# Kernel optimization log

Measured on AMD Instinct MI355X. Metric: run time of the kernel, lower is better.

The kernel has to match this reference:

```python
import jax, jax.numpy as jnp
import numpy as np

B, T, EMB, HS = 4, 4096, 1024, 64
BASE = 10000.0


def rope_angles(T, hs, base=BASE):
    # theta_i = base^(-2i/hs), freqs[t, i] = t * theta_i  -> (T, hs//2)
    inv = 1.0 / (base ** (2.0 * jnp.arange(hs // 2, dtype=jnp.float32) / hs))
    return jnp.arange(T, dtype=jnp.float32)[:, None] * inv[None, :]


def apply_rope(x, cos, sin):
    # x: (B, T, D); pairs are interleaved (even, odd) like torch.view_as_complex
    xr = x.reshape(*x.shape[:-1], -1, 2)
    xe, xo = xr[..., 0], xr[..., 1]
    re = xe * cos - xo * sin
    im = xe * sin + xo * cos
    return jnp.stack([re, im], axis=-1).reshape(x.shape)


def setup_inputs() -> dict:
    key = jax.random.key(0)
    kx, kq, kk, kv = jax.random.split(key, 4)
    s = 1.0 / np.sqrt(EMB)
    return {
        "x": jax.random.normal(kx, (B, T, EMB), jnp.float32),
        "Wq": jax.random.normal(kq, (HS, EMB), jnp.float32) * s,
        "Wk": jax.random.normal(kk, (HS, EMB), jnp.float32) * s,
        "Wv": jax.random.normal(kv, (HS, EMB), jnp.float32) * s,
    }


def reference(x, Wq, Wk, Wv):
    Tlen = x.shape[1]
    ang = rope_angles(Tlen, HS)          # (T, HS//2)
    cos, sin = jnp.cos(ang), jnp.sin(ang)
    q = x @ Wq.T                          # (B, T, HS)
    k = x @ Wk.T
    v = x @ Wv.T
    q = apply_rope(q, cos, sin)
    k = apply_rope(k, cos, sin)
    scores = jnp.einsum("bqd,bkd->bqk", q, k) * (HS ** -0.5)
    causal = jnp.tril(jnp.ones((Tlen, Tlen), dtype=bool))
    scores = jnp.where(causal[None], scores, -jnp.inf)
    w = jax.nn.softmax(scores, axis=-1)   # dropout in eval mode: identity
    return jnp.einsum("bqk,bkd->bqd", w, v)
```

## Files before the change

kernel.cpp:

```cpp
#include <hip/hip_runtime.h>

typedef __bf16 bf16x8 __attribute__((ext_vector_type(8)));
typedef __bf16 bf16x4 __attribute__((ext_vector_type(4)));
typedef float f32x4 __attribute__((ext_vector_type(4)));
typedef float f32x16 __attribute__((ext_vector_type(16)));
typedef unsigned int u32;

#define T_LEN 4096

__device__ __forceinline__ f32x4 mfma16(bf16x8 a, bf16x8 b, f32x4 c) {
    return __builtin_amdgcn_mfma_f32_16x16x32_bf16(a, b, c, 0, 0, 0);
}
__device__ __forceinline__ f32x16 mfma32(bf16x8 a, bf16x8 b, f32x16 c) {
    return __builtin_amdgcn_mfma_f32_32x32x16_bf16(a, b, c, 0, 0, 0);
}
__device__ __forceinline__ u32 packbf(float lo, float hi) {
    union { __bf16 e[2]; u32 w; } u;
    u.e[0] = (__bf16)lo; u.e[1] = (__bf16)hi;
    return u.w;
}
__device__ __forceinline__ f32x16 zero16() {
    f32x16 z;
    #pragma unroll
    for (int i = 0; i < 16; i++) z[i] = 0.f;
    return z;
}

__global__ __launch_bounds__(256) void convert_w_kernel(
    const float* __restrict__ Wq, const float* __restrict__ Wk,
    const float* __restrict__ Wv, __bf16* __restrict__ wb)
{
    int i = blockIdx.x * 256 + threadIdx.x;
    int m = i >> 14, off = (i & 16383) << 2;
    const float* s = (m == 0 ? Wq : (m == 1 ? Wk : Wv)) + off;
    float4 f = *(const float4*)s;
    bf16x4 h = { (__bf16)f.x, (__bf16)f.y, (__bf16)f.z, (__bf16)f.w };
    *(bf16x4*)(wb + (m << 16) + off) = h;
}

__global__ __launch_bounds__(512, 2) void proj_kernel(
    const float* __restrict__ x, const __bf16* __restrict__ wb,
    __bf16* __restrict__ qfb, __bf16* __restrict__ kfb, __bf16* __restrict__ vfb)
{
    __shared__ __bf16 xs[2][32][72];
    __shared__ __bf16 wl[2][192][72];
    const int tid  = threadIdx.x;
    const int wave = tid >> 6, lane = tid & 63;
    const int l15 = lane & 15, l4 = lane >> 4;
    const int wm = wave >> 2, wn = wave & 3;
    const size_t m0 = (size_t)blockIdx.x * 32;
    const int xrow = tid >> 4, xc4 = (tid & 15) * 4;
    const int wrow = tid >> 3, wcp = (tid & 7) * 8;

    f32x4 acc[3];
    #pragma unroll
    for (int bn = 0; bn < 3; bn++) acc[bn] = (f32x4){0.f, 0.f, 0.f, 0.f};

    const float* xsrc = x + (m0 + xrow) * 1024 + xc4;

    float4 rx;
    bf16x8 rw[3];

    rx = *(const float4*)(xsrc);
    #pragma unroll
    for (int j = 0; j < 3; j++)
        rw[j] = *(const bf16x8*)(wb + (size_t)(wrow + j * 64) * 1024 + wcp);
    {
        bf16x4 hx = {(__bf16)rx.x, (__bf16)rx.y, (__bf16)rx.z, (__bf16)rx.w};
        *(bf16x4*)&xs[0][xrow][xc4] = hx;
        #pragma unroll
        for (int j = 0; j < 3; j++)
            *(bf16x8*)&wl[0][wrow + j * 64][wcp] = rw[j];
    }
    __syncthreads();

    for (int t = 0; t < 16; t++) {
        const int cur = t & 1;
        if (t < 15) {
            const int k0 = (t + 1) * 64;
            rx = *(const float4*)(xsrc + k0);
            #pragma unroll
            for (int j = 0; j < 3; j++)
                rw[j] = *(const bf16x8*)(wb + (size_t)(wrow + j * 64) * 1024 + k0 + wcp);
        }
        bf16x8 af[2], bfr[3][2];
        #pragma unroll
        for (int c = 0; c < 2; c++)
            af[c] = *(const bf16x8*)&xs[cur][wm * 16 + l15][c * 32 + l4 * 8];
        #pragma unroll
        for (int nf = 0; nf < 3; nf++)
            #pragma unroll
            for (int c = 0; c < 2; c++)
                bfr[nf][c] = *(const bf16x8*)&wl[cur][wn * 48 + nf * 16 + l15][c * 32 + l4 * 8];
        #pragma unroll
        for (int nf = 0; nf < 3; nf++)
            #pragma unroll
            for (int c = 0; c < 2; c++)
                acc[nf] = mfma16(af[c], bfr[nf][c], acc[nf]);
        if (t < 15) {
            bf16x4 hx = {(__bf16)rx.x, (__bf16)rx.y, (__bf16)rx.z, (__bf16)rx.w};
            *(bf16x4*)&xs[cur ^ 1][xrow][xc4] = hx;
            #pragma unroll
            for (int j = 0; j < 3; j++)
                *(bf16x8*)&wl[cur ^ 1][wrow + j * 64][wcp] = rw[j];
        }
        __syncthreads();
    }

    #pragma unroll
    for (int nf = 0; nf < 3; nf++) {
        int n = wn * 48 + nf * 16 + l15;
        #pragma unroll
        for (int r = 0; r < 4; r++) {
            size_t mrow = m0 + wm * 16 + l4 * 4 + r;
            float val = acc[nf][r];
            float partner = __shfl_xor(val, 1);
            const int bb = (int)(mrow >> 12);
            const int tq = (int)(mrow & 4095);
            const size_t bbase = (size_t)bb * 262144;
            if (n < 128) {
                int i = (n & 63) >> 1;
                float inv = __builtin_exp2f((float)i * (-13.287712379549449f / 32.f));
                float ang = (float)tq * inv;
                float sn, cs;
                __sincosf(ang, &sn, &cs);
                float res = (n & 1) ? (partner * sn + val * cs)
                                    : (val * cs - partner * sn);
                if (n < 64) {
                    res *= 0.180336884f;
                    int d = n;
                    size_t idx = bbase + (size_t)(tq >> 5) * 2048 + (d >> 4) * 512
                               + ((tq & 31) + ((d >> 3) & 1) * 32) * 8 + (d & 7);
                    qfb[idx] = (__bf16)res;
                } else {
                    int d = n - 64, rr = tq & 31;
                    int l31i = ((rr >> 2) & 1) * 16 + ((rr >> 4) & 1) * 8
                             + ((rr >> 3) & 1) * 4 + (rr & 3);
                    size_t idx = bbase + (size_t)(tq >> 5) * 2048 + (d >> 4) * 512
                               + (l31i + ((d >> 3) & 1) * 32) * 8 + (d & 7);
                    kfb[idx] = (__bf16)res;
                }
            } else {
                int d = n - 128;
                int cc = ((d >> 5) << 1) | ((tq & 31) >> 4);
                size_t idx = bbase + (size_t)(tq >> 5) * 2048 + cc * 512
                           + ((d & 31) + ((tq >> 3) & 1) * 32) * 8 + (tq & 7);
                vfb[idx] = (__bf16)val;
            }
        }
    }
}

__global__ __launch_bounds__(1024) void flash_kernel(
    const __bf16* __restrict__ qfb, const __bf16* __restrict__ kfb,
    const __bf16* __restrict__ vfb, float* __restrict__ out)
{
    __shared__ float ods[16][32][36];
    __shared__ float mls[2][16][32];

    const int tid = threadIdx.x;
    const int wave = tid >> 6, lane = tid & 63;
    const int l31 = lane & 31, h = lane >> 5;
    const int xcd = blockIdx.x & 7;
    const int b = xcd >> 1;
    const int p = ((blockIdx.x >> 3) << 1) | (xcd & 1);

    const __bf16* qb_b = qfb + (size_t)b * 262144;
    const __bf16* kb_b = kfb + (size_t)b * 262144;
    const __bf16* vb_b = vfb + (size_t)b * 262144;

    #pragma unroll 1
    for (int half = 0; half < 2; half++) {
        const int jt = half ? p : 127 - p;
        const int q0 = jt * 32;
        const int qg = q0 + l31;

        const __bf16* qp = qb_b + (size_t)jt * 2048 + lane * 8;
        bf16x8 qf[4];
        #pragma unroll
        for (int dc = 0; dc < 4; dc++) qf[dc] = *(const bf16x8*)(qp + dc * 512);

        float m = 16.f, l = 0.f;
        f32x16 o0 = zero16(), o1 = zero16();
        const int nt = jt + 1;

        #pragma unroll 1
        for (int kt = wave; kt < nt; kt += 16) {
            const int kc0 = kt << 5;
            const __bf16* kr = kb_b + (size_t)kt * 2048 + lane * 8;
            bf16x8 kf0 = *(const bf16x8*)(kr);
            bf16x8 kf1 = *(const bf16x8*)(kr + 512);
            bf16x8 kf2 = *(const bf16x8*)(kr + 1024);
            bf16x8 kf3 = *(const bf16x8*)(kr + 1536);
            const __bf16* vr = vb_b + (size_t)kt * 2048 + lane * 8;
            bf16x8 vf00 = *(const bf16x8*)(vr);
            bf16x8 vf01 = *(const bf16x8*)(vr + 512);
            bf16x8 vf10 = *(const bf16x8*)(vr + 1024);
            bf16x8 vf11 = *(const bf16x8*)(vr + 1536);
            f32x16 s = zero16();
            __builtin_amdgcn_s_setprio(1);
            s = mfma32(kf0, qf[0], s);
            s = mfma32(kf1, qf[1], s);
            s = mfma32(kf2, qf[2], s);
            s = mfma32(kf3, qf[3], s);
            __builtin_amdgcn_s_setprio(0);
            if (kt == jt) {
                #pragma unroll
                for (int r = 0; r < 16; r++) {
                    int pioff = ((r >> 2) & 1) * 16 + 8 * h + (r >> 3) * 4 + (r & 3);
                    if (kc0 + pioff > qg) s[r] = -1e30f;
                }
            }
            float tm[8];
            #pragma unroll
            for (int i = 0; i < 8; i++) tm[i] = fmaxf(s[2 * i], s[2 * i + 1]);
            #pragma unroll
            for (int i = 0; i < 4; i++) tm[i] = fmaxf(tm[i], tm[i + 4]);
            float tmax = fmaxf(fmaxf(tm[0], tm[1]), fmaxf(tm[2], tm[3]));
            float ts[4] = {0.f, 0.f, 0.f, 0.f};
            #pragma unroll
            for (int r = 0; r < 16; r++) {
                float e = __builtin_exp2f(s[r] - m);
                s[r] = e;
                ts[r & 3] += e;
            }
            float lsum = (ts[0] + ts[1]) + (ts[2] + ts[3]);
            float lsum_p = __shfl_xor(lsum, 32);
            float tmax_p = __shfl_xor(tmax, 32);
            union { u32 w[4]; bf16x8 v; } pf[2];
            #pragma unroll
            for (int cg = 0; cg < 2; cg++) {
                pf[cg].w[0] = packbf(s[4 * cg + 0],  s[4 * cg + 1]);
                pf[cg].w[1] = packbf(s[4 * cg + 2],  s[4 * cg + 3]);
                pf[cg].w[2] = packbf(s[4 * cg + 8],  s[4 * cg + 9]);
                pf[cg].w[3] = packbf(s[4 * cg + 10], s[4 * cg + 11]);
            }
            __builtin_amdgcn_s_setprio(1);
            o0 = mfma32(vf00, pf[0].v, o0);
            o0 = mfma32(vf01, pf[1].v, o0);
            o1 = mfma32(vf10, pf[0].v, o1);
            o1 = mfma32(vf11, pf[1].v, o1);
            __builtin_amdgcn_s_setprio(0);
            l += lsum + lsum_p;
            float tmx = fmaxf(tmax, tmax_p);
            if (!__all(tmx <= m + 8.f)) {
                const float mnew = fmaxf(m, tmx);
                const float alpha = __builtin_exp2f(m - mnew);
                m = mnew;
                l *= alpha;
                #pragma unroll
                for (int r = 0; r < 16; r++) { o0[r] *= alpha; o1[r] *= alpha; }
            }
        }

        const int q = tid >> 5, dcm = tid & 31;
        #pragma unroll
        for (int c2 = 0; c2 < 4; c2++) {
            f32x4 w0 = {o0[4 * c2], o0[4 * c2 + 1], o0[4 * c2 + 2], o0[4 * c2 + 3]};
            *(f32x4*)&ods[wave][l31][8 * c2 + 4 * h] = w0;
        }
        if (h == 0) {
            mls[0][wave][l31] = (wave < nt) ? m : -1e30f;
            mls[1][wave][l31] = l;
        }
        __syncthreads();
        float M = -1e30f;
        #pragma unroll
        for (int s2 = 0; s2 < 16; s2++) M = fmaxf(M, mls[0][s2][q]);
        float w16[16], L = 0.f;
        #pragma unroll
        for (int s2 = 0; s2 < 16; s2++) {
            float ws = __builtin_exp2f(mls[0][s2][q] - M);
            w16[s2] = ws;
            L += ws * mls[1][s2][q];
        }
        const float invL = 1.f / L;
        float accA = 0.f;
        #pragma unroll
        for (int s2 = 0; s2 < 16; s2++) accA += w16[s2] * ods[s2][q][dcm];
        out[((size_t)b * T_LEN + q0 + q) * 64 + dcm] = accA * invL;
        __syncthreads();
        #pragma unroll
        for (int c2 = 0; c2 < 4; c2++) {
            f32x4 w1 = {o1[4 * c2], o1[4 * c2 + 1], o1[4 * c2 + 2], o1[4 * c2 + 3]};
            *(f32x4*)&ods[wave][l31][8 * c2 + 4 * h] = w1;
        }
        __syncthreads();
        float accB = 0.f;
        #pragma unroll
        for (int s2 = 0; s2 < 16; s2++) accB += w16[s2] * ods[s2][q][dcm];
        out[((size_t)b * T_LEN + q0 + q) * 64 + 32 + dcm] = accB * invL;
        __syncthreads();
    }
}

extern "C" void kernel_launch(void* const* d_in, const int* in_sizes, int n_in,
                              void* d_out, int out_size, void* d_ws, size_t ws_size,
                              hipStream_t stream)
{
    const float* x  = (const float*)d_in[0];
    const float* Wq = (const float*)d_in[1];
    const float* Wk = (const float*)d_in[2];
    const float* Wv = (const float*)d_in[3];
    float* out = (float*)d_out;

    __bf16* qfb = (__bf16*)d_ws;
    __bf16* kfb = qfb + 1048576;
    __bf16* vfb = kfb + 1048576;
    __bf16* wb  = vfb + 1048576;

    convert_w_kernel<<<192, 256, 0, stream>>>(Wq, Wk, Wv, wb);
    proj_kernel<<<512, 512, 0, stream>>>(x, wb, qfb, kfb, vfb);
    flash_kernel<<<256, 1024, 0, stream>>>(qfb, kfb, vfb, out);
}
```

Measured before the change: 62.49 us.

## Stage projection outputs in LDS for vectorized stores; deepen x prefetch

The projection kernel now writes its rotated Q/K and V values into a shared-memory staging buffer, which reuses the tile buffers. After a barrier, each thread copies them to global memory as contiguous 4-element bf16 stores, replacing scattered 2-byte stores. The x loads are also prefetched two k-steps ahead instead of one, to hide more global latency. The cost is an extra barrier, extra register pressure from the second prefetch register, and some index arithmetic.

```diff
diff --git a/kernel.cpp b/kernel.cpp
--- a/kernel.cpp
+++ b/kernel.cpp
@@ -42,8 +42,11 @@
     const float* __restrict__ x, const __bf16* __restrict__ wb,
     __bf16* __restrict__ qfb, __bf16* __restrict__ kfb, __bf16* __restrict__ vfb)
 {
-    __shared__ __bf16 xs[2][32][72];
-    __shared__ __bf16 wl[2][192][72];
+    __shared__ __bf16 smem[4608 + 27648];
+    __bf16 (*xs)[32][72]  = (__bf16(*)[32][72])smem;
+    __bf16 (*wl)[192][72] = (__bf16(*)[192][72])(smem + 4608);
+    __bf16* stage = smem;
+
     const int tid  = threadIdx.x;
     const int wave = tid >> 6, lane = tid & 63;
     const int l15 = lane & 15, l4 = lane >> 4;
@@ -58,27 +61,28 @@
 
     const float* xsrc = x + (m0 + xrow) * 1024 + xc4;
 
-    float4 rx;
+    float4 rxA, rxB;
     bf16x8 rw[3];
 
-    rx = *(const float4*)(xsrc);
-    #pragma unroll
-    for (int j = 0; j < 3; j++)
-        rw[j] = *(const bf16x8*)(wb + (size_t)(wrow + j * 64) * 1024 + wcp);
     {
-        bf16x4 hx = {(__bf16)rx.x, (__bf16)rx.y, (__bf16)rx.z, (__bf16)rx.w};
+        float4 r0 = *(const float4*)(xsrc);
+        bf16x4 hx = {(__bf16)r0.x, (__bf16)r0.y, (__bf16)r0.z, (__bf16)r0.w};
         *(bf16x4*)&xs[0][xrow][xc4] = hx;
         #pragma unroll
-        for (int j = 0; j < 3; j++)
+        for (int j = 0; j < 3; j++) {
+            rw[j] = *(const bf16x8*)(wb + (size_t)(wrow + j * 64) * 1024 + wcp);
             *(bf16x8*)&wl[0][wrow + j * 64][wcp] = rw[j];
+        }
+        rxA = *(const float4*)(xsrc + 64);
     }
     __syncthreads();
 
     for (int t = 0; t < 16; t++) {
         const int cur = t & 1;
+        if (t < 14)
+            rxB = *(const float4*)(xsrc + (t + 2) * 64);
         if (t < 15) {
             const int k0 = (t + 1) * 64;
-            rx = *(const float4*)(xsrc + k0);
             #pragma unroll
             for (int j = 0; j < 3; j++)
                 rw[j] = *(const bf16x8*)(wb + (size_t)(wrow + j * 64) * 1024 + k0 + wcp);
@@ -98,30 +102,29 @@
             for (int c = 0; c < 2; c++)
                 acc[nf] = mfma16(af[c], bfr[nf][c], acc[nf]);
         if (t < 15) {
-            bf16x4 hx = {(__bf16)rx.x, (__bf16)rx.y, (__bf16)rx.z, (__bf16)rx.w};
+            bf16x4 hx = {(__bf16)rxA.x, (__bf16)rxA.y, (__bf16)rxA.z, (__bf16)rxA.w};
             *(bf16x4*)&xs[cur ^ 1][xrow][xc4] = hx;
             #pragma unroll
             for (int j = 0; j < 3; j++)
                 *(bf16x8*)&wl[cur ^ 1][wrow + j * 64][wcp] = rw[j];
         }
-        __syncthreads();
-    }
-
+        rxA = rxB;
+        __syncthreads();
+    }
+
+    const int tq0 = (int)(m0 & 4095);
     #pragma unroll
     for (int nf = 0; nf < 3; nf++) {
         int n = wn * 48 + nf * 16 + l15;
         #pragma unroll
         for (int r = 0; r < 4; r++) {
-            size_t mrow = m0 + wm * 16 + l4 * 4 + r;
+            int row = wm * 16 + l4 * 4 + r;
             float val = acc[nf][r];
             float partner = __shfl_xor(val, 1);
-            const int bb = (int)(mrow >> 12);
-            const int tq = (int)(mrow & 4095);
-            const size_t bbase = (size_t)bb * 262144;
             if (n < 128) {
                 int i = (n & 63) >> 1;
-                float inv = __builtin_exp2f((float)i * (-13.287712379549449f / 32.f));
-                float ang = (float)tq * inv;
+                float ang = (float)(tq0 + row)
+                          * __builtin_exp2f((float)i * (-13.287712379549449f / 32.f));
                 float sn, cs;
                 __sincosf(ang, &sn, &cs);
                 float res = (n & 1) ? (partner * sn + val * cs)
@@ -129,25 +132,34 @@
                 if (n < 64) {
                     res *= 0.180336884f;
                     int d = n;
-                    size_t idx = bbase + (size_t)(tq >> 5) * 2048 + (d >> 4) * 512
-                               + ((tq & 31) + ((d >> 3) & 1) * 32) * 8 + (d & 7);
-                    qfb[idx] = (__bf16)res;
+                    stage[(d >> 4) * 512 + (row + ((d >> 3) & 1) * 32) * 8 + (d & 7)]
+                        = (__bf16)res;
                 } else {
-                    int d = n - 64, rr = tq & 31;
-                    int l31i = ((rr >> 2) & 1) * 16 + ((rr >> 4) & 1) * 8
-                             + ((rr >> 3) & 1) * 4 + (rr & 3);
-                    size_t idx = bbase + (size_t)(tq >> 5) * 2048 + (d >> 4) * 512
-                               + (l31i + ((d >> 3) & 1) * 32) * 8 + (d & 7);
-                    kfb[idx] = (__bf16)res;
+                    int d = n - 64;
+                    int l31i = ((row >> 2) & 1) * 16 + ((row >> 4) & 1) * 8
+                             + ((row >> 3) & 1) * 4 + (row & 3);
+                    stage[2048 + (d >> 4) * 512
+                          + (l31i + ((d >> 3) & 1) * 32) * 8 + (d & 7)] = (__bf16)res;
                 }
             } else {
                 int d = n - 128;
-                int cc = ((d >> 5) << 1) | ((tq & 31) >> 4);
-                size_t idx = bbase + (size_t)(tq >> 5) * 2048 + cc * 512
-                           + ((d & 31) + ((tq >> 3) & 1) * 32) * 8 + (tq & 7);
-                vfb[idx] = (__bf16)val;
-            }
-        }
+                int cc = ((d >> 5) << 1) | ((row & 31) >> 4);
+                stage[4096 + cc * 512
+                      + ((d & 31) + ((row >> 3) & 1) * 32) * 8 + (row & 7)]
+                    = (__bf16)val;
+            }
+        }
+    }
+    __syncthreads();
+    {
+        const size_t bbase = (size_t)(m0 >> 12) * 262144;
+        const size_t tbase = (size_t)((m0 & 4095) >> 5) * 2048;
+        bf16x4 q4 = *(const bf16x4*)&stage[tid * 4];
+        bf16x4 k4 = *(const bf16x4*)&stage[2048 + tid * 4];
+        bf16x4 v4 = *(const bf16x4*)&stage[4096 + tid * 4];
+        *(bf16x4*)(qfb + bbase + tbase + tid * 4) = q4;
+        *(bf16x4*)(kfb + bbase + tbase + tid * 4) = k4;
+        *(bf16x4*)(vfb + bbase + tbase + tid * 4) = v4;
     }
 }
 
```

Result: faster. 54.13 us (-13.4%).

## Fuse QKV projection and flash attention into one kernel with grid barrier

Applied to the files above, without the earlier changes.

Merges the projection kernel and the flash-attention kernel into a single 256-block persistent kernel. Each block first projects 64 rows, staging the RoPE'd Q/K/V tiles in shared memory so they can be written out with coalesced vector stores. A global atomic counter barrier then synchronizes all blocks before the attention phase. This removes one kernel launch and its tail. In exchange it relies on all 256 blocks being co-resident, and the projection phase runs at a different block size and occupancy than before.

```diff
diff --git a/kernel.cpp b/kernel.cpp
--- a/kernel.cpp
+++ b/kernel.cpp
@@ -28,8 +28,10 @@
 
 __global__ __launch_bounds__(256) void convert_w_kernel(
     const float* __restrict__ Wq, const float* __restrict__ Wk,
-    const float* __restrict__ Wv, __bf16* __restrict__ wb)
+    const float* __restrict__ Wv, __bf16* __restrict__ wb, u32* bar)
 {
+    if (blockIdx.x == 0 && threadIdx.x == 0)
+        __hip_atomic_store(bar, 0u, __ATOMIC_RELAXED, __HIP_MEMORY_SCOPE_AGENT);
     int i = blockIdx.x * 256 + threadIdx.x;
     int m = i >> 14, off = (i & 16383) << 2;
     const float* s = (m == 0 ? Wq : (m == 1 ? Wk : Wv)) + off;
@@ -38,259 +40,285 @@
     *(bf16x4*)(wb + (m << 16) + off) = h;
 }
 
-__global__ __launch_bounds__(512, 2) void proj_kernel(
+__global__ __launch_bounds__(1024) void fused_kernel(
     const float* __restrict__ x, const __bf16* __restrict__ wb,
-    __bf16* __restrict__ qfb, __bf16* __restrict__ kfb, __bf16* __restrict__ vfb)
+    __bf16* __restrict__ qfb, __bf16* __restrict__ kfb, __bf16* __restrict__ vfb,
+    float* __restrict__ out, u32* bar)
 {
-    __shared__ __bf16 xs[2][32][72];
-    __shared__ __bf16 wl[2][192][72];
-    const int tid  = threadIdx.x;
+    __shared__ float smemf[19456];
+    __bf16* sb = (__bf16*)smemf;
+    __bf16 (*xs)[64][72]  = (__bf16(*)[64][72])sb;
+    __bf16 (*wl)[192][72] = (__bf16(*)[192][72])(sb + 9216);
+    __bf16* stage = sb;
+    float (*ods)[32][36] = (float(*)[32][36])smemf;
+    float (*mls)[16][32] = (float(*)[16][32])(smemf + 18432);
+
+    const int tid = threadIdx.x;
     const int wave = tid >> 6, lane = tid & 63;
     const int l15 = lane & 15, l4 = lane >> 4;
-    const int wm = wave >> 2, wn = wave & 3;
-    const size_t m0 = (size_t)blockIdx.x * 32;
-    const int xrow = tid >> 4, xc4 = (tid & 15) * 4;
-    const int wrow = tid >> 3, wcp = (tid & 7) * 8;
-
-    f32x4 acc[3];
-    #pragma unroll
-    for (int bn = 0; bn < 3; bn++) acc[bn] = (f32x4){0.f, 0.f, 0.f, 0.f};
-
-    const float* xsrc = x + (m0 + xrow) * 1024 + xc4;
-
-    float4 rx;
-    bf16x8 rw[3];
-
-    rx = *(const float4*)(xsrc);
-    #pragma unroll
-    for (int j = 0; j < 3; j++)
-        rw[j] = *(const bf16x8*)(wb + (size_t)(wrow + j * 64) * 1024 + wcp);
+    const int l31 = lane & 31, h = lane >> 5;
+    const int blk = blockIdx.x;
+
     {
-        bf16x4 hx = {(__bf16)rx.x, (__bf16)rx.y, (__bf16)rx.z, (__bf16)rx.w};
-        *(bf16x4*)&xs[0][xrow][xc4] = hx;
+        const int wm = wave >> 2;
+        const int wn = wave & 3;
+        const size_t m0 = (size_t)blk * 64;
+        const int xrow = tid >> 4, xc4 = (tid & 15) * 4;
+        const int wrow = tid >> 3, wcp = (tid & 7) * 8;
+
+        f32x4 acc[3];
         #pragma unroll
-        for (int j = 0; j < 3; j++)
-            *(bf16x8*)&wl[0][wrow + j * 64][wcp] = rw[j];
+        for (int nf = 0; nf < 3; nf++) acc[nf] = (f32x4){0.f, 0.f, 0.f, 0.f};
+
+        const float* xsrc = x + (m0 + xrow) * 1024 + xc4;
+
+        float4 rx;
+        bf16x8 rw0, rw1;
+
+        rx = *(const float4*)(xsrc);
+        rw0 = *(const bf16x8*)(wb + (size_t)wrow * 1024 + wcp);
+        if (tid < 512)
+            rw1 = *(const bf16x8*)(wb + (size_t)(128 + wrow) * 1024 + wcp);
+        {
+            bf16x4 hx = {(__bf16)rx.x, (__bf16)rx.y, (__bf16)rx.z, (__bf16)rx.w};
+            *(bf16x4*)&xs[0][xrow][xc4] = hx;
+            *(bf16x8*)&wl[0][wrow][wcp] = rw0;
+            if (tid < 512) *(bf16x8*)&wl[0][128 + wrow][wcp] = rw1;
+        }
+        __syncthreads();
+
+        for (int t = 0; t < 16; t++) {
+            const int cur = t & 1;
+            if (t < 15) {
+                const int k0 = (t + 1) * 64;
+                rx = *(const float4*)(xsrc + k0);
+                rw0 = *(const bf16x8*)(wb + (size_t)wrow * 1024 + k0 + wcp);
+                if (tid < 512)
+                    rw1 = *(const bf16x8*)(wb + (size_t)(128 + wrow) * 1024 + k0 + wcp);
+            }
+            bf16x8 af[2];
+            #pragma unroll
+            for (int c = 0; c < 2; c++)
+                af[c] = *(const bf16x8*)&xs[cur][wm * 16 + l15][c * 32 + l4 * 8];
+            #pragma unroll
+            for (int nf = 0; nf < 3; nf++) {
+                #pragma unroll
+                for (int c = 0; c < 2; c++) {
+                    bf16x8 bw = *(const bf16x8*)&wl[cur][(wn * 3 + nf) * 16 + l15][c * 32 + l4 * 8];
+                    acc[nf] = mfma16(af[c], bw, acc[nf]);
+                }
+            }
+            if (t < 15) {
+                bf16x4 hx = {(__bf16)rx.x, (__bf16)rx.y, (__bf16)rx.z, (__bf16)rx.w};
+                *(bf16x4*)&xs[cur ^ 1][xrow][xc4] = hx;
+                *(bf16x8*)&wl[cur ^ 1][wrow][wcp] = rw0;
+                if (tid < 512) *(bf16x8*)&wl[cur ^ 1][128 + wrow][wcp] = rw1;
+            }
+            __syncthreads();
+        }
+
+        const int tq0 = (int)(m0 & 4095);
+        #pragma unroll
+        for (int nf = 0; nf < 3; nf++) {
+            int n = (wn * 3 + nf) * 16 + l15;
+            #pragma unroll
+            for (int r = 0; r < 4; r++) {
+                int row64 = wm * 16 + l4 * 4 + r;
+                int tile = row64 >> 5, rr = row64 & 31;
+                int tb = tile * 6144;
+                float val = acc[nf][r];
+                float partner = __shfl_xor(val, 1);
+                if (n < 128) {
+                    int i = (n & 63) >> 1;
+                    float ang = (float)(tq0 + row64)
+                              * __builtin_exp2f((float)i * (-13.287712379549449f / 32.f));
+                    float sn, cs;
+                    __sincosf(ang, &sn, &cs);
+                    float res = (n & 1) ? (partner * sn + val * cs)
+                                        : (val * cs - partner * sn);
+                    if (n < 64) {
+                        res *= 0.180336884f;
+                        int d = n;
+                        stage[tb + (d >> 4) * 512
+                              + (rr + ((d >> 3) & 1) * 32) * 8 + (d & 7)] = (__bf16)res;
+                    } else {
+                        int d = n - 64;
+                        int l31i = ((rr >> 2) & 1) * 16 + ((rr >> 4) & 1) * 8
+                                 + ((rr >> 3) & 1) * 4 + (rr & 3);
+                        stage[tb + 2048 + (d >> 4) * 512
+                              + (l31i + ((d >> 3) & 1) * 32) * 8 + (d & 7)] = (__bf16)res;
+                    }
+                } else {
+                    int d = n - 128;
+                    int cc = ((d >> 5) << 1) | (rr >> 4);
+                    stage[tb + 4096 + cc * 512
+                          + ((d & 31) + ((rr >> 3) & 1) * 32) * 8 + (rr & 7)]
+                        = (__bf16)val;
+                }
+            }
+        }
+        __syncthreads();
+        {
+            const size_t bbase = (size_t)(m0 >> 12) * 262144;
+            const size_t tbase = (size_t)((m0 & 4095) >> 5) * 2048;
+            const int tile = tid >> 9;
+            const int inner = (tid & 511) * 4;
+            const int tb = tile * 6144;
+            const size_t go = bbase + tbase + (size_t)tile * 2048 + inner;
+            bf16x4 q4 = *(const bf16x4*)&stage[tb + inner];
+            bf16x4 k4 = *(const bf16x4*)&stage[tb + 2048 + inner];
+            bf16x4 v4 = *(const bf16x4*)&stage[tb + 4096 + inner];
+            *(bf16x4*)(qfb + go) = q4;
+            *(bf16x4*)(kfb + go) = k4;
+            *(bf16x4*)(vfb + go) = v4;
+        }
+    }
+
+    __threadfence();
+    __syncthreads();
+    if (tid == 0) {
+        __hip_atomic_fetch_add(bar, 1u, __ATOMIC_ACQ_REL, __HIP_MEMORY_SCOPE_AGENT);
+        u32 v;
+        do {
+            __builtin_amdgcn_s_sleep(16);
+            v = __hip_atomic_load(bar, __ATOMIC_ACQUIRE, __HIP_MEMORY_SCOPE_AGENT);
+        } while (v < 256u);
     }
     __syncthreads();
-
-    for (int t = 0; t < 16; t++) {
-        const int cur = t & 1;
-        if (t < 15) {
-            const int k0 = (t + 1) * 64;
-            rx = *(const float4*)(xsrc + k0);
-            #pragma unroll
-            for (int j = 0; j < 3; j++)
-                rw[j] = *(const bf16x8*)(wb + (size_t)(wrow + j * 64) * 1024 + k0 + wcp);
-        }
-        bf16x8 af[2], bfr[3][2];
-        #pragma unroll
-        for (int c = 0; c < 2; c++)
-            af[c] = *(const bf16x8*)&xs[cur][wm * 16 + l15][c * 32 + l4 * 8];
-        #pragma unroll
-        for (int nf = 0; nf < 3; nf++)
-            #pragma unroll
-            for (int c = 0; c < 2; c++)
-                bfr[nf][c] = *(const bf16x8*)&wl[cur][wn * 48 + nf * 16 + l15][c * 32 + l4 * 8];
-        #pragma unroll
-        for (int nf = 0; nf < 3; nf++)
-            #pragma unroll
-            for (int c = 0; c < 2; c++)
-                acc[nf] = mfma16(af[c], bfr[nf][c], acc[nf]);
-        if (t < 15) {
-            bf16x4 hx = {(__bf16)rx.x, (__bf16)rx.y, (__bf16)rx.z, (__bf16)rx.w};
-            *(bf16x4*)&xs[cur ^ 1][xrow][xc4] = hx;
-            #pragma unroll
-            for (int j = 0; j < 3; j++)
-                *(bf16x8*)&wl[cur ^ 1][wrow + j * 64][wcp] = rw[j];
-        }
-        __syncthreads();
-    }
-
-    #pragma unroll
-    for (int nf = 0; nf < 3; nf++) {
-        int n = wn * 48 + nf * 16 + l15;
-        #pragma unroll
-        for (int r = 0; r < 4; r++) {
-            size_t mrow = m0 + wm * 16 + l4 * 4 + r;
-            float val = acc[nf][r];
-            float partner = __shfl_xor(val, 1);
-            const int bb = (int)(mrow >> 12);
-            const int tq = (int)(mrow & 4095);
-            const size_t bbase = (size_t)bb * 262144;
-            if (n < 128) {
-                int i = (n & 63) >> 1;
-                float inv = __builtin_exp2f((float)i * (-13.287712379549449f / 32.f));
-                float ang = (float)tq * inv;
-                float sn, cs;
-                __sincosf(ang, &sn, &cs);
-                float res = (n & 1) ? (partner * sn + val * cs)
-                                    : (val * cs - partner * sn);
-                if (n < 64) {
-                    res *= 0.180336884f;
-                    int d = n;
-                    size_t idx = bbase + (size_t)(tq >> 5) * 2048 + (d >> 4) * 512
-                               + ((tq & 31) + ((d >> 3) & 1) * 32) * 8 + (d & 7);
-                    qfb[idx] = (__bf16)res;
-                } else {
-                    int d = n - 64, rr = tq & 31;
-                    int l31i = ((rr >> 2) & 1) * 16 + ((rr >> 4) & 1) * 8
-                             + ((rr >> 3) & 1) * 4 + (rr & 3);
-                    size_t idx = bbase + (size_t)(tq >> 5) * 2048 + (d >> 4) * 512
-                               + (l31i + ((d >> 3) & 1) * 32) * 8 + (d & 7);
-                    kfb[idx] = (__bf16)res;
-                }
-            } else {
-                int d = n - 128;
-                int cc = ((d >> 5) << 1) | ((tq & 31) >> 4);
-                size_t idx = bbase + (size_t)(tq >> 5) * 2048 + cc * 512
-                           + ((d & 31) + ((tq >> 3) & 1) * 32) * 8 + (tq & 7);
-                vfb[idx] = (__bf16)val;
-            }
-        }
-    }
-}
-
-__global__ __launch_bounds__(1024) void flash_kernel(
-    const __bf16* __restrict__ qfb, const __bf16* __restrict__ kfb,
-    const __bf16* __restrict__ vfb, float* __restrict__ out)
-{
-    __shared__ float ods[16][32][36];
-    __shared__ float mls[2][16][32];
-
-    const int tid = threadIdx.x;
-    const int wave = tid >> 6, lane = tid & 63;
-    const int l31 = lane & 31, h = lane >> 5;
-    const int xcd = blockIdx.x & 7;
-    const int b = xcd >> 1;
-    const int p = ((blockIdx.x >> 3) << 1) | (xcd & 1);
-
-    const __bf16* qb_b = qfb + (size_t)b * 262144;
-    const __bf16* kb_b = kfb + (size_t)b * 262144;
-    const __bf16* vb_b = vfb + (size_t)b * 262144;
-
-    #pragma unroll 1
-    for (int half = 0; half < 2; half++) {
-        const int jt = half ? p : 127 - p;
-        const int q0 = jt * 32;
-        const int qg = q0 + l31;
-
-        const __bf16* qp = qb_b + (size_t)jt * 2048 + lane * 8;
-        bf16x8 qf[4];
-        #pragma unroll
-        for (int dc = 0; dc < 4; dc++) qf[dc] = *(const bf16x8*)(qp + dc * 512);
-
-        float m = 16.f, l = 0.f;
-        f32x16 o0 = zero16(), o1 = zero16();
-        const int nt = jt + 1;
+    __threadfence();
+
+    {
+        const int xcd = blk & 7;
+        const int b = xcd >> 1;
+        const int p = ((blk >> 3) << 1) | (xcd & 1);
+
+        const __bf16* qb_b = qfb + (size_t)b * 262144;
+        const __bf16* kb_b = kfb + (size_t)b * 262144;
+        const __bf16* vb_b = vfb + (size_t)b * 262144;
 
         #pragma unroll 1
-        for (int kt = wave; kt < nt; kt += 16) {
-            const int kc0 = kt << 5;
-            const __bf16* kr = kb_b + (size_t)kt * 2048 + lane * 8;
-            bf16x8 kf0 = *(const bf16x8*)(kr);
-            bf16x8 kf1 = *(const bf16x8*)(kr + 512);
-            bf16x8 kf2 = *(const bf16x8*)(kr + 1024);
-            bf16x8 kf3 = *(const bf16x8*)(kr + 1536);
-            const __bf16* vr = vb_b + (size_t)kt * 2048 + lane * 8;
-            bf16x8 vf00 = *(const bf16x8*)(vr);
-            bf16x8 vf01 = *(const bf16x8*)(vr + 512);
-            bf16x8 vf10 = *(const bf16x8*)(vr + 1024);
-            bf16x8 vf11 = *(const bf16x8*)(vr + 1536);
-            f32x16 s = zero16();
-            __builtin_amdgcn_s_setprio(1);
-            s = mfma32(kf0, qf[0], s);
-            s = mfma32(kf1, qf[1], s);
-            s = mfma32(kf2, qf[2], s);
-            s = mfma32(kf3, qf[3], s);
-            __builtin_amdgcn_s_setprio(0);
-            if (kt == jt) {
+        for (int half = 0; half < 2; half++) {
+            const int jt = half ? p : 127 - p;
+            const int q0 = jt * 32;
+            const int qg = q0 + l31;
+
+            const __bf16* qp = qb_b + (size_t)jt * 2048 + lane * 8;
+            bf16x8 qf[4];
+            #pragma unroll
+            for (int dc = 0; dc < 4; dc++) qf[dc] = *(const bf16x8*)(qp + dc * 512);
+
+            float m = 16.f, l = 0.f;
+            f32x16 o0 = zero16(), o1 = zero16();
+            const int nt = jt + 1;
+
+            #pragma unroll 1
+            for (int kt = wave; kt < nt; kt += 16) {
+                const int kc0 = kt << 5;
+                const __bf16* kr = kb_b + (size_t)kt * 2048 + lane * 8;
+                bf16x8 kf0 = *(const bf16x8*)(kr);
+                bf16x8 kf1 = *(const bf16x8*)(kr + 512);
+                bf16x8 kf2 = *(const bf16x8*)(kr + 1024);
+                bf16x8 kf3 = *(const bf16x8*)(kr + 1536);
+                const __bf16* vr = vb_b + (size_t)kt * 2048 + lane * 8;
+                bf16x8 vf00 = *(const bf16x8*)(vr);
+                bf16x8 vf01 = *(const bf16x8*)(vr + 512);
+                bf16x8 vf10 = *(const bf16x8*)(vr + 1024);
+                bf16x8 vf11 = *(const bf16x8*)(vr + 1536);
+                f32x16 s = zero16();
+                __builtin_amdgcn_s_setprio(1);
+                s = mfma32(kf0, qf[0], s);
+                s = mfma32(kf1, qf[1], s);
+                s = mfma32(kf2, qf[2], s);
+                s = mfma32(kf3, qf[3], s);
+                __builtin_amdgcn_s_setprio(0);
+                if (kt == jt) {
+                    #pragma unroll
+                    for (int r = 0; r < 16; r++) {
+                        int pioff = ((r >> 2) & 1) * 16 + 8 * h + (r >> 3) * 4 + (r & 3);
+                        if (kc0 + pioff > qg) s[r] = -1e30f;
+                    }
+                }
+                float tm[8];
+                #pragma unroll
+                for (int i = 0; i < 8; i++) tm[i] = fmaxf(s[2 * i], s[2 * i + 1]);
+                #pragma unroll
+                for (int i = 0; i < 4; i++) tm[i] = fmaxf(tm[i], tm[i + 4]);
+                float tmax = fmaxf(fmaxf(tm[0], tm[1]), fmaxf(tm[2], tm[3]));
+                float ts[4] = {0.f, 0.f, 0.f, 0.f};
                 #pragma unroll
                 for (int r = 0; r < 16; r++) {
-                    int pioff = ((r >> 2) & 1) * 16 + 8 * h + (r >> 3) * 4 + (r & 3);
-                    if (kc0 + pioff > qg) s[r] = -1e30f;
-                }
-            }
-            float tm[8];
-            #pragma unroll
-            for (int i = 0; i < 8; i++) tm[i] = fmaxf(s[2 * i], s[2 * i + 1]);
-            #pragma unroll
-            for (int i = 0; i < 4; i++) tm[i] = fmaxf(tm[i], tm[i + 4]);
-            float tmax = fmaxf(fmaxf(tm[0], tm[1]), fmaxf(tm[2], tm[3]));
-            float ts[4] = {0.f, 0.f, 0.f, 0.f};
-            #pragma unroll
-            for (int r = 0; r < 16; r++) {
-                float e = __builtin_exp2f(s[r] - m);
-                s[r] = e;
-                ts[r & 3] += e;
-            }
-            float lsum = (ts[0] + ts[1]) + (ts[2] + ts[3]);
-            float lsum_p = __shfl_xor(lsum, 32);
-            float tmax_p = __shfl_xor(tmax, 32);
-            union { u32 w[4]; bf16x8 v; } pf[2];
-            #pragma unroll
-            for (int cg = 0; cg < 2; cg++) {
-                pf[cg].w[0] = packbf(s[4 * cg + 0],  s[4 * cg + 1]);
-                pf[cg].w[1] = packbf(s[4 * cg + 2],  s[4 * cg + 3]);
-                pf[cg].w[2] = packbf(s[4 * cg + 8],  s[4 * cg + 9]);
-                pf[cg].w[3] = packbf(s[4 * cg + 10], s[4 * cg + 11]);
-            }
-            __builtin_amdgcn_s_setprio(1);
-            o0 = mfma32(vf00, pf[0].v, o0);
-            o0 = mfma32(vf01, pf[1].v, o0);
-            o1 = mfma32(vf10, pf[0].v, o1);
-            o1 = mfma32(vf11, pf[1].v, o1);
-            __builtin_amdgcn_s_setprio(0);
-            l += lsum + lsum_p;
-            float tmx = fmaxf(tmax, tmax_p);
-            if (!__all(tmx <= m + 8.f)) {
-                const float mnew = fmaxf(m, tmx);
-                const float alpha = __builtin_exp2f(m - mnew);
-                m = mnew;
-                l *= alpha;
-                #pragma unroll
-                for (int r = 0; r < 16; r++) { o0[r] *= alpha; o1[r] *= alpha; }
-            }
-        }
-
-        const int q = tid >> 5, dcm = tid & 31;
-        #pragma unroll
-        for (int c2 = 0; c2 < 4; c2++) {
-            f32x4 w0 = {o0[4 * c2], o0[4 * c2 + 1], o0[4 * c2 + 2], o0[4 * c2 + 3]};
-            *(f32x4*)&ods[wave][l31][8 * c2 + 4 * h] = w0;
-        }
-        if (h == 0) {
-            mls[0][wave][l31] = (wave < nt) ? m : -1e30f;
-            mls[1][wave][l31] = l;
-        }
-        __syncthreads();
-        float M = -1e30f;
-        #pragma unroll
-        for (int s2 = 0; s2 < 16; s2++) M = fmaxf(M, mls[0][s2][q]);
-        float w16[16], L = 0.f;
-        #pragma unroll
-        for (int s2 = 0; s2 < 16; s2++) {
-            float ws = __builtin_exp2f(mls[0][s2][q] - M);
-            w16[s2] = ws;
-            L += ws * mls[1][s2][q];
-        }
-        const float invL = 1.f / L;
-        float accA = 0.f;
-        #pragma unroll
-        for (int s2 = 0; s2 < 16; s2++) accA += w16[s2] * ods[s2][q][dcm];
-        out[((size_t)b * T_LEN + q0 + q) * 64 + dcm] = accA * invL;
-        __syncthreads();
-        #pragma unroll
-        for (int c2 = 0; c2 < 4; c2++) {
-            f32x4 w1 = {o1[4 * c2], o1[4 * c2 + 1], o1[4 * c2 + 2], o1[4 * c2 + 3]};
-            *(f32x4*)&ods[wave][l31][8 * c2 + 4 * h] = w1;
-        }
-        __syncthreads();
-        float accB = 0.f;
-        #pragma unroll
-        for (int s2 = 0; s2 < 16; s2++) accB += w16[s2] * ods[s2][q][dcm];
-        out[((size_t)b * T_LEN + q0 + q) * 64 + 32 + dcm] = accB * invL;
-        __syncthreads();
+                    float e = __builtin_exp2f(s[r] - m);
+                    s[r] = e;
+                    ts[r & 3] += e;
+                }
+                float lsum = (ts[0] + ts[1]) + (ts[2] + ts[3]);
+                float lsum_p = __shfl_xor(lsum, 32);
+                float tmax_p = __shfl_xor(tmax, 32);
+                union { u32 w[4]; bf16x8 v; } pf[2];
+                #pragma unroll
+                for (int cg = 0; cg < 2; cg++) {
+                    pf[cg].w[0] = packbf(s[4 * cg + 0],  s[4 * cg + 1]);
+                    pf[cg].w[1] = packbf(s[4 * cg + 2],  s[4 * cg + 3]);
+                    pf[cg].w[2] = packbf(s[4 * cg + 8],  s[4 * cg + 9]);
+                    pf[cg].w[3] = packbf(s[4 * cg + 10], s[4 * cg + 11]);
+                }
+                __builtin_amdgcn_s_setprio(1);
+                o0 = mfma32(vf00, pf[0].v, o0);
+                o0 = mfma32(vf01, pf[1].v, o0);
+                o1 = mfma32(vf10, pf[0].v, o1);
+                o1 = mfma32(vf11, pf[1].v, o1);
+                __builtin_amdgcn_s_setprio(0);
+                l += lsum + lsum_p;
+                float tmx = fmaxf(tmax, tmax_p);
+                if (!__all(tmx <= m + 8.f)) {
+                    const float mnew = fmaxf(m, tmx);
+                    const float alpha = __builtin_exp2f(m - mnew);
+                    m = mnew;
+                    l *= alpha;
+                    #pragma unroll
+                    for (int r = 0; r < 16; r++) { o0[r] *= alpha; o1[r] *= alpha; }
+                }
+            }
+
+            const int q = tid >> 5, dcm = tid & 31;
+            #pragma unroll
+            for (int c2 = 0; c2 < 4; c2++) {
+                f32x4 w0 = {o0[4 * c2], o0[4 * c2 + 1], o0[4 * c2 + 2], o0[4 * c2 + 3]};
+                *(f32x4*)&ods[wave][l31][8 * c2 + 4 * h] = w0;
+            }
+            if (h == 0) {
+                mls[0][wave][l31] = (wave < nt) ? m : -1e30f;
+                mls[1][wave][l31] = l;
+            }
+            __syncthreads();
+            float M = -1e30f;
+            #pragma unroll
+            for (int s2 = 0; s2 < 16; s2++) M = fmaxf(M, mls[0][s2][q]);
+            float w16[16], L = 0.f;
+            #pragma unroll
+            for (int s2 = 0; s2 < 16; s2++) {
+                float ws = __builtin_exp2f(mls[0][s2][q] - M);
+                w16[s2] = ws;
+                L += ws * mls[1][s2][q];
+            }
+            const float invL = 1.f / L;
+            float accA = 0.f;
+            #pragma unroll
+            for (int s2 = 0; s2 < 16; s2++) accA += w16[s2] * ods[s2][q][dcm];
+            out[((size_t)b * T_LEN + q0 + q) * 64 + dcm] = accA * invL;
+            __syncthreads();
+            #pragma unroll
+            for (int c2 = 0; c2 < 4; c2++) {
+                f32x4 w1 = {o1[4 * c2], o1[4 * c2 + 1], o1[4 * c2 + 2], o1[4 * c2 + 3]};
+                *(f32x4*)&ods[wave][l31][8 * c2 + 4 * h] = w1;
+            }
+            __syncthreads();
+            float accB = 0.f;
+            #pragma unroll
+            for (int s2 = 0; s2 < 16; s2++) accB += w16[s2] * ods[s2][q][dcm];
+            out[((size_t)b * T_LEN + q0 + q) * 64 + 32 + dcm] = accB * invL;
+            __syncthreads();
+        }
     }
 }
 
@@ -308,8 +336,8 @@
     __bf16* kfb = qfb + 1048576;
     __bf16* vfb = kfb + 1048576;
     __bf16* wb  = vfb + 1048576;
-
-    convert_w_kernel<<<192, 256, 0, stream>>>(Wq, Wk, Wv, wb);
-    proj_kernel<<<512, 512, 0, stream>>>(x, wb, qfb, kfb, vfb);
-    flash_kernel<<<256, 1024, 0, stream>>>(qfb, kfb, vfb, out);
-}
+    u32*    bar = (u32*)(wb + 196608);
+
+    convert_w_kernel<<<192, 256, 0, stream>>>(Wq, Wk, Wv, wb, bar);
+    fused_kernel<<<256, 1024, 0, stream>>>(x, wb, qfb, kfb, vfb, out, bar);
+}
```

New measurement: 204.6 us. 227% more time.

## Split projection scatter into row-major stores plus a separate relayout kernel

Applied to the files above, without the earlier changes.

The projection kernel now writes Q, K and V in plain row-major layout instead of scattering each element into the MFMA-fragment layout. A new relayout kernel stages 32-row tiles in shared memory and writes the fragment layout with contiguous 16-byte stores. The aim is to replace scattered 2-byte global writes with coalesced ones. In exchange it adds a kernel launch and an extra round trip through global memory for the Q, K and V buffers.

```diff
diff --git a/kernel.cpp b/kernel.cpp
--- a/kernel.cpp
+++ b/kernel.cpp
@@ -40,7 +40,7 @@
 
 __global__ __launch_bounds__(512, 2) void proj_kernel(
     const float* __restrict__ x, const __bf16* __restrict__ wb,
-    __bf16* __restrict__ qfb, __bf16* __restrict__ kfb, __bf16* __restrict__ vfb)
+    __bf16* __restrict__ qr, __bf16* __restrict__ kr, __bf16* __restrict__ vr)
 {
     __shared__ __bf16 xs[2][32][72];
     __shared__ __bf16 wl[2][192][72];
@@ -115,39 +115,67 @@
             size_t mrow = m0 + wm * 16 + l4 * 4 + r;
             float val = acc[nf][r];
             float partner = __shfl_xor(val, 1);
-            const int bb = (int)(mrow >> 12);
-            const int tq = (int)(mrow & 4095);
-            const size_t bbase = (size_t)bb * 262144;
             if (n < 128) {
                 int i = (n & 63) >> 1;
+                int t = (int)(mrow & 4095);
                 float inv = __builtin_exp2f((float)i * (-13.287712379549449f / 32.f));
-                float ang = (float)tq * inv;
+                float ang = (float)t * inv;
                 float sn, cs;
                 __sincosf(ang, &sn, &cs);
                 float res = (n & 1) ? (partner * sn + val * cs)
                                     : (val * cs - partner * sn);
                 if (n < 64) {
                     res *= 0.180336884f;
-                    int d = n;
-                    size_t idx = bbase + (size_t)(tq >> 5) * 2048 + (d >> 4) * 512
-                               + ((tq & 31) + ((d >> 3) & 1) * 32) * 8 + (d & 7);
-                    qfb[idx] = (__bf16)res;
+                    qr[mrow * 64 + n] = (__bf16)res;
                 } else {
-                    int d = n - 64, rr = tq & 31;
-                    int l31i = ((rr >> 2) & 1) * 16 + ((rr >> 4) & 1) * 8
-                             + ((rr >> 3) & 1) * 4 + (rr & 3);
-                    size_t idx = bbase + (size_t)(tq >> 5) * 2048 + (d >> 4) * 512
-                               + (l31i + ((d >> 3) & 1) * 32) * 8 + (d & 7);
-                    kfb[idx] = (__bf16)res;
+                    kr[mrow * 64 + (n - 64)] = (__bf16)res;
                 }
             } else {
-                int d = n - 128;
-                int cc = ((d >> 5) << 1) | ((tq & 31) >> 4);
-                size_t idx = bbase + (size_t)(tq >> 5) * 2048 + cc * 512
-                           + ((d & 31) + ((tq >> 3) & 1) * 32) * 8 + (tq & 7);
-                vfb[idx] = (__bf16)val;
-            }
-        }
+                vr[mrow * 64 + (n - 128)] = (__bf16)val;
+            }
+        }
+    }
+}
+
+__global__ __launch_bounds__(256) void relayout_kernel(
+    const __bf16* __restrict__ qr, const __bf16* __restrict__ kr,
+    const __bf16* __restrict__ vr,
+    __bf16* __restrict__ qfb, __bf16* __restrict__ kfb, __bf16* __restrict__ vfb)
+{
+    __shared__ __bf16 stage[6144];
+    const int tid = threadIdx.x;
+    const int blk = blockIdx.x;
+    const int tl = tid >> 3;
+    const int d0 = (tid & 7) * 8;
+    const size_t gsrc = (size_t)blk * 32 * 64 + (size_t)tl * 64 + d0;
+
+    bf16x8 q8 = *(const bf16x8*)(qr + gsrc);
+    bf16x8 k8 = *(const bf16x8*)(kr + gsrc);
+    bf16x8 v8 = *(const bf16x8*)(vr + gsrc);
+
+    {
+        int qdst = (d0 >> 4) * 512 + (tl + ((d0 >> 3) & 1) * 32) * 8;
+        *(bf16x8*)&stage[qdst] = q8;
+    }
+    {
+        int l31i = ((tl >> 2) & 1) * 16 + ((tl >> 4) & 1) * 8
+                 + ((tl >> 3) & 1) * 4 + (tl & 3);
+        int kdst = 2048 + (d0 >> 4) * 512 + (l31i + ((d0 >> 3) & 1) * 32) * 8;
+        *(bf16x8*)&stage[kdst] = k8;
+    }
+    #pragma unroll
+    for (int j = 0; j < 8; j++) {
+        int d = d0 + j;
+        int cc = ((d >> 5) << 1) | (tl >> 4);
+        int vdst = 4096 + cc * 512 + ((d & 31) + ((tl >> 3) & 1) * 32) * 8 + (tl & 7);
+        stage[vdst] = v8[j];
+    }
+    __syncthreads();
+    {
+        const size_t go = (size_t)blk * 2048 + tid * 8;
+        *(bf16x8*)(qfb + go) = *(const bf16x8*)&stage[tid * 8];
+        *(bf16x8*)(kfb + go) = *(const bf16x8*)&stage[2048 + tid * 8];
+        *(bf16x8*)(vfb + go) = *(const bf16x8*)&stage[4096 + tid * 8];
     }
 }
 
@@ -187,16 +215,16 @@
         #pragma unroll 1
         for (int kt = wave; kt < nt; kt += 16) {
             const int kc0 = kt << 5;
-            const __bf16* kr = kb_b + (size_t)kt * 2048 + lane * 8;
-            bf16x8 kf0 = *(const bf16x8*)(kr);
-            bf16x8 kf1 = *(const bf16x8*)(kr + 512);
-            bf16x8 kf2 = *(const bf16x8*)(kr + 1024);
-            bf16x8 kf3 = *(const bf16x8*)(kr + 1536);
-            const __bf16* vr = vb_b + (size_t)kt * 2048 + lane * 8;
-            bf16x8 vf00 = *(const bf16x8*)(vr);
-            bf16x8 vf01 = *(const bf16x8*)(vr + 512);
-            bf16x8 vf10 = *(const bf16x8*)(vr + 1024);
-            bf16x8 vf11 = *(const bf16x8*)(vr + 1536);
+            const __bf16* kp = kb_b + (size_t)kt * 2048 + lane * 8;
+            bf16x8 kf0 = *(const bf16x8*)(kp);
+            bf16x8 kf1 = *(const bf16x8*)(kp + 512);
+            bf16x8 kf2 = *(const bf16x8*)(kp + 1024);
+            bf16x8 kf3 = *(const bf16x8*)(kp + 1536);
+            const __bf16* vp = vb_b + (size_t)kt * 2048 + lane * 8;
+            bf16x8 vf00 = *(const bf16x8*)(vp);
+            bf16x8 vf01 = *(const bf16x8*)(vp + 512);
+            bf16x8 vf10 = *(const bf16x8*)(vp + 1024);
+            bf16x8 vf11 = *(const bf16x8*)(vp + 1536);
             f32x16 s = zero16();
             __builtin_amdgcn_s_setprio(1);
             s = mfma32(kf0, qf[0], s);
@@ -308,8 +336,12 @@
     __bf16* kfb = qfb + 1048576;
     __bf16* vfb = kfb + 1048576;
     __bf16* wb  = vfb + 1048576;
+    __bf16* qr  = wb  + 196608;
+    __bf16* kr  = qr  + 1048576;
+    __bf16* vr  = kr  + 1048576;
 
     convert_w_kernel<<<192, 256, 0, stream>>>(Wq, Wk, Wv, wb);
-    proj_kernel<<<512, 512, 0, stream>>>(x, wb, qfb, kfb, vfb);
+    proj_kernel<<<512, 512, 0, stream>>>(x, wb, qr, kr, vr);
+    relayout_kernel<<<512, 256, 0, stream>>>(qr, kr, vr, qfb, kfb, vfb);
     flash_kernel<<<256, 1024, 0, stream>>>(qfb, kfb, vfb, out);
 }
```

Result: faster. 59.74 us (-4.4%).
